# Kernel tuning notes

Measured on AMD Instinct MI355X. Metric: run time of the kernel, lower is better.

## Reference

```python
import jax, jax.numpy as jnp
import numpy as np

COMPLEXES = 2048
RESX = 16
RESY = 16
RATE = 16
FEAT = 64


def setup_inputs() -> dict:
    key = jax.random.key(0)
    k1, k2, k3 = jax.random.split(key, 3)
    P = RATE * RATE  # samples per complex
    map_ = jax.random.normal(k1, (COMPLEXES, RESY, RESX, FEAT), dtype=jnp.float32)
    u = jax.random.uniform(k2, (COMPLEXES, P), dtype=jnp.float32)
    v = jax.random.uniform(k3, (COMPLEXES, P), dtype=jnp.float32)
    return {"map": map_, "u": u, "v": v}


def reference(map, u, v):
    # map: [complexes, resy, resx, feat]; u, v: [complexes, P] in [0,1]
    C, H, W, F = map.shape
    x = u * (W - 1)
    y = v * (H - 1)
    x0 = jnp.clip(jnp.floor(x).astype(jnp.int32), 0, W - 2)
    y0 = jnp.clip(jnp.floor(y).astype(jnp.int32), 0, H - 2)
    fx = (x - x0.astype(x.dtype))[..., None]  # [C, P, 1]
    fy = (y - y0.astype(y.dtype))[..., None]
    cidx = jnp.arange(C)[:, None]  # [C, 1] broadcast over samples
    g00 = map[cidx, y0, x0]          # [C, P, F]
    g01 = map[cidx, y0, x0 + 1]
    g10 = map[cidx, y0 + 1, x0]
    g11 = map[cidx, y0 + 1, x0 + 1]
    top = g00 * (1.0 - fx) + g01 * fx
    bot = g10 * (1.0 - fx) + g11 * fx
    return top * (1.0 - fy) + bot * fy  # [C, P, F]
```

## Files before the change

### kernel.cpp

```cpp
#include <hip/hip_runtime.h>

constexpr int C_ = 2048;
constexpr int H_ = 16;
constexpr int W_ = 16;
constexpr int F_ = 64;
constexpr int P_ = 256;
constexpr int MAP4 = H_ * W_ * F_ / 4;
constexpr int BLK = 1024;
constexpr int NBLOCKS = 256;
constexpr int NC = C_ / NBLOCKS;
constexpr int ITERS = 4;

typedef __attribute__((address_space(3))) uint32_t lds_u32;
typedef const __attribute__((address_space(1))) uint32_t glb_u32;
using f32x4 = __attribute__((ext_vector_type(4))) float;

__global__ __launch_bounds__(BLK, 4) void ngf_fetch_kernel(
    const float* __restrict__ map_,
    const float* __restrict__ u_,
    const float* __restrict__ v_,
    float* __restrict__ out_) {
  __shared__ float4 smap[2][MAP4];
  __shared__ float4 s_w[2][P_];
  __shared__ int    s_ix[2][P_];

  const int b = blockIdx.x;
  const int tid = threadIdx.x;
  const int f = tid & 15;
  const int sbase = tid >> 4;

  auto cidx = [&](int i) { return i * NBLOCKS + b; };

  auto stage = [&](int c, int buf) {
    const float4* __restrict__ g =
        (const float4*)(map_ + (size_t)c * (H_ * W_ * F_));
#pragma unroll
    for (int k = 0; k < MAP4 / BLK; ++k) {
      __builtin_amdgcn_global_load_lds((glb_u32*)(g + k * BLK + tid),
                                       (lds_u32*)(&smap[buf][k * BLK + tid]),
                                       16, 0, 0);
    }
  };

  auto coeffs = [&](int c, int buf) {
    if (tid < P_) {
      const float x = u_[(size_t)c * P_ + tid] * (float)(W_ - 1);
      const float y = v_[(size_t)c * P_ + tid] * (float)(H_ - 1);
      int x0 = (int)floorf(x);
      int y0 = (int)floorf(y);
      x0 = x0 < 0 ? 0 : (x0 > W_ - 2 ? W_ - 2 : x0);
      y0 = y0 < 0 ? 0 : (y0 > H_ - 2 ? H_ - 2 : y0);
      const float fx = x - (float)x0;
      const float fy = y - (float)y0;
      const float wx0 = 1.0f - fx;
      const float wy0 = 1.0f - fy;
      s_w[buf][tid] = make_float4(wx0 * wy0, fx * wy0, wx0 * fy, fx * fy);
      s_ix[buf][tid] = (y0 * W_ + x0) * (F_ / 4);
    }
  };

  auto compute_store = [&](int c, int buf) {
    float4 w[ITERS];
    int ix[ITERS];
#pragma unroll
    for (int it = 0; it < ITERS; ++it) {
      const int s = it * (BLK / 16) + sbase;
      w[it] = s_w[buf][s];
      ix[it] = s_ix[buf][s] + f;
    }
    float4* __restrict__ gout = (float4*)(out_ + (size_t)c * (P_ * F_));
#pragma unroll
    for (int it = 0; it < ITERS; ++it) {
      const int s = it * (BLK / 16) + sbase;
      const float4 g00 = smap[buf][ix[it]];
      const float4 g01 = smap[buf][ix[it] + (F_ / 4)];
      const float4 g10 = smap[buf][ix[it] + W_ * (F_ / 4)];
      const float4 g11 = smap[buf][ix[it] + (W_ + 1) * (F_ / 4)];

      f32x4 r;
      r.x = g00.x * w[it].x + g01.x * w[it].y + g10.x * w[it].z + g11.x * w[it].w;
      r.y = g00.y * w[it].x + g01.y * w[it].y + g10.y * w[it].z + g11.y * w[it].w;
      r.z = g00.z * w[it].x + g01.z * w[it].y + g10.z * w[it].z + g11.z * w[it].w;
      r.w = g00.w * w[it].x + g01.w * w[it].y + g10.w * w[it].z + g11.w * w[it].w;

      __builtin_nontemporal_store(r, (f32x4*)(gout + s * (F_ / 4) + f));
    }
  };

  int i = 0, cur = 0;
  stage(cidx(0), 0);
  coeffs(cidx(0), 0);
  __syncthreads();

  if (b & 1) {
    compute_store(cidx(0), 0);
    __syncthreads();
    stage(cidx(1), 1);
    coeffs(cidx(1), 1);
    __syncthreads();
    i = 1;
    cur = 1;
  }

  for (; i < NC; ++i) {
    const int nxt = cur ^ 1;
    if (i + 1 < NC) {
      stage(cidx(i + 1), nxt);
      coeffs(cidx(i + 1), nxt);
    }
    compute_store(cidx(i), cur);

    __syncthreads();
    cur = nxt;
  }
}

extern "C" void kernel_launch(void* const* d_in, const int* in_sizes, int n_in,
                              void* d_out, int out_size, void* d_ws, size_t ws_size,
                              hipStream_t stream) {
  const float* map_ = (const float*)d_in[0];
  const float* u_   = (const float*)d_in[1];
  const float* v_   = (const float*)d_in[2];
  float* out_ = (float*)d_out;

  ngf_fetch_kernel<<<NBLOCKS, BLK, 0, stream>>>(map_, u_, v_, out_);
}
```

Measured before the change: 241.2 us.

## Precompute all sample coefficients upfront and pipeline map staging with manual waitcnt barrier

Computes the fractional offsets and base indices for every complex a block handles in a single upfront pass, instead of once per iteration. It stores two floats per sample rather than four weights, and the compute step rebuilds the bilinear weights in factored form. The main loop drops the odd/even block staggering and swaps __syncthreads for sched barriers plus an explicit s_waitcnt vmcnt(4) and s_barrier. The aim is to overlap the next map's global-to-LDS load with compute while removing per-iteration coefficient work. The risk is the hand-tuned vmcnt count, which must match the number of outstanding stores and loads for the loop to be correct.

```diff
diff --git a/kernel.cpp b/kernel.cpp
--- a/kernel.cpp
+++ b/kernel.cpp
@@ -21,15 +21,13 @@
     const float* __restrict__ v_,
     float* __restrict__ out_) {
   __shared__ float4 smap[2][MAP4];
-  __shared__ float4 s_w[2][P_];
-  __shared__ int    s_ix[2][P_];
+  __shared__ float2 s_cf[NC * P_];
+  __shared__ int    s_ix[NC * P_];
 
   const int b = blockIdx.x;
   const int tid = threadIdx.x;
   const int f = tid & 15;
   const int sbase = tid >> 4;
-
-  auto cidx = [&](int i) { return i * NBLOCKS + b; };
 
   auto stage = [&](int c, int buf) {
     const float4* __restrict__ g =
@@ -42,32 +40,17 @@
     }
   };
 
-  auto coeffs = [&](int c, int buf) {
-    if (tid < P_) {
-      const float x = u_[(size_t)c * P_ + tid] * (float)(W_ - 1);
-      const float y = v_[(size_t)c * P_ + tid] * (float)(H_ - 1);
-      int x0 = (int)floorf(x);
-      int y0 = (int)floorf(y);
-      x0 = x0 < 0 ? 0 : (x0 > W_ - 2 ? W_ - 2 : x0);
-      y0 = y0 < 0 ? 0 : (y0 > H_ - 2 ? H_ - 2 : y0);
-      const float fx = x - (float)x0;
-      const float fy = y - (float)y0;
-      const float wx0 = 1.0f - fx;
-      const float wy0 = 1.0f - fy;
-      s_w[buf][tid] = make_float4(wx0 * wy0, fx * wy0, wx0 * fy, fx * fy);
-      s_ix[buf][tid] = (y0 * W_ + x0) * (F_ / 4);
-    }
-  };
-
-  auto compute_store = [&](int c, int buf) {
-    float4 w[ITERS];
+  auto compute_store = [&](int i, int buf) {
+    const int base = i * P_;
+    float2 cf[ITERS];
     int ix[ITERS];
 #pragma unroll
     for (int it = 0; it < ITERS; ++it) {
       const int s = it * (BLK / 16) + sbase;
-      w[it] = s_w[buf][s];
-      ix[it] = s_ix[buf][s] + f;
+      cf[it] = s_cf[base + s];
+      ix[it] = s_ix[base + s] + f;
     }
+    const int c = i * NBLOCKS + b;
     float4* __restrict__ gout = (float4*)(out_ + (size_t)c * (P_ * F_));
 #pragma unroll
     for (int it = 0; it < ITERS; ++it) {
@@ -77,42 +60,53 @@
       const float4 g10 = smap[buf][ix[it] + W_ * (F_ / 4)];
       const float4 g11 = smap[buf][ix[it] + (W_ + 1) * (F_ / 4)];
 
+      const float wx1 = cf[it].x, wx0 = 1.0f - cf[it].x;
+      const float wy1 = cf[it].y, wy0 = 1.0f - cf[it].y;
+
       f32x4 r;
-      r.x = g00.x * w[it].x + g01.x * w[it].y + g10.x * w[it].z + g11.x * w[it].w;
-      r.y = g00.y * w[it].x + g01.y * w[it].y + g10.y * w[it].z + g11.y * w[it].w;
-      r.z = g00.z * w[it].x + g01.z * w[it].y + g10.z * w[it].z + g11.z * w[it].w;
-      r.w = g00.w * w[it].x + g01.w * w[it].y + g10.w * w[it].z + g11.w * w[it].w;
+      r.x = (g00.x * wx0 + g01.x * wx1) * wy0 + (g10.x * wx0 + g11.x * wx1) * wy1;
+      r.y = (g00.y * wx0 + g01.y * wx1) * wy0 + (g10.y * wx0 + g11.y * wx1) * wy1;
+      r.z = (g00.z * wx0 + g01.z * wx1) * wy0 + (g10.z * wx0 + g11.z * wx1) * wy1;
+      r.w = (g00.w * wx0 + g01.w * wx1) * wy0 + (g10.w * wx0 + g11.w * wx1) * wy1;
 
       __builtin_nontemporal_store(r, (f32x4*)(gout + s * (F_ / 4) + f));
     }
   };
 
-  int i = 0, cur = 0;
-  stage(cidx(0), 0);
-  coeffs(cidx(0), 0);
+  stage(b, 0);
+#pragma unroll
+  for (int g = tid; g < NC * P_; g += BLK) {
+    const int i = g >> 8;
+    const int p = g & (P_ - 1);
+    const int c = i * NBLOCKS + b;
+    const float x = u_[(size_t)c * P_ + p] * (float)(W_ - 1);
+    const float y = v_[(size_t)c * P_ + p] * (float)(H_ - 1);
+    int x0 = (int)floorf(x);
+    int y0 = (int)floorf(y);
+    x0 = x0 < 0 ? 0 : (x0 > W_ - 2 ? W_ - 2 : x0);
+    y0 = y0 < 0 ? 0 : (y0 > H_ - 2 ? H_ - 2 : y0);
+    s_cf[g] = make_float2(x - (float)x0, y - (float)y0);
+    s_ix[g] = (y0 * W_ + x0) * (F_ / 4);
+  }
   __syncthreads();
 
-  if (b & 1) {
-    compute_store(cidx(0), 0);
-    __syncthreads();
-    stage(cidx(1), 1);
-    coeffs(cidx(1), 1);
-    __syncthreads();
-    i = 1;
-    cur = 1;
-  }
+  int cur = 0;
+  for (int i = 0; i < NC - 1; ++i) {
+    const int nxt = cur ^ 1;
 
-  for (; i < NC; ++i) {
-    const int nxt = cur ^ 1;
-    if (i + 1 < NC) {
-      stage(cidx(i + 1), nxt);
-      coeffs(cidx(i + 1), nxt);
-    }
-    compute_store(cidx(i), cur);
+    stage((i + 1) * NBLOCKS + b, nxt);
+    __builtin_amdgcn_sched_barrier(0);
 
-    __syncthreads();
+    compute_store(i, cur);
+    __builtin_amdgcn_sched_barrier(0);
+
+    asm volatile("s_waitcnt vmcnt(4) lgkmcnt(0)" ::: "memory");
+    __builtin_amdgcn_s_barrier();
+    __builtin_amdgcn_sched_barrier(0);
+
     cur = nxt;
   }
+  compute_store(NC - 1, cur);
 }
 
 extern "C" void kernel_launch(void* const* d_in, const int* in_sizes, int n_in,
```

Measured after the change: 240.3 us. No clear change (-0.4%).
